# Kernel tuning notes

Measured on AMD Instinct MI355X. Metric: run time of the kernel, lower is better.

## Reference

```python
import jax, jax.numpy as jnp
import numpy as np
import math

HIDDEN = 1024
HEADS = 16
D_K = HIDDEN // HEADS
EPS = 1e-5


def gelu_tanh(x):
    c = math.sqrt(2.0 / math.pi)
    return 0.5 * x * (1.0 + jnp.tanh(c * (x + 0.044715 * x ** 3)))


def layer_norm(x, gamma, beta):
    mu = jnp.mean(x, axis=-1, keepdims=True)
    var = jnp.mean((x - mu) ** 2, axis=-1, keepdims=True)
    return (x - mu) * jax.lax.rsqrt(var + EPS) * gamma + beta


def setup_inputs() -> dict:
    key = jax.random.key(0)
    ks = jax.random.split(key, 12)
    s = 1.0 / math.sqrt(HIDDEN)
    s4 = 1.0 / math.sqrt(4 * HIDDEN)
    inp = {
        "x": jax.random.normal(ks[0], (2, 2048, HIDDEN), dtype=jnp.float32),
        # attention linears, stored as (in, out) so y = x @ W + b
        "Wq": jax.random.uniform(ks[1], (HIDDEN, HIDDEN), minval=-s, maxval=s),
        "bq": jax.random.uniform(ks[2], (HIDDEN,), minval=-s, maxval=s),
        "Wv": jax.random.uniform(ks[3], (HIDDEN, HIDDEN), minval=-s, maxval=s),
        "bv": jax.random.uniform(ks[4], (HIDDEN,), minval=-s, maxval=s),
        "Wo": jax.random.uniform(ks[5], (HIDDEN, HIDDEN), minval=-s, maxval=s),
        "bo": jax.random.uniform(ks[6], (HIDDEN,), minval=-s, maxval=s),
        # feed-forward
        "W1": jax.random.uniform(ks[7], (HIDDEN, 4 * HIDDEN), minval=-s, maxval=s),
        "b1": jax.random.uniform(ks[8], (4 * HIDDEN,), minval=-s, maxval=s),
        "W2": jax.random.uniform(ks[9], (4 * HIDDEN, HIDDEN), minval=-s4, maxval=s4),
        "b2": jax.random.uniform(ks[10], (HIDDEN,), minval=-s4, maxval=s4),
        # layer norms
        "g1": jnp.ones((HIDDEN,), jnp.float32),
        "beta1": jnp.zeros((HIDDEN,), jnp.float32),
        "g2": jnp.ones((HIDDEN,), jnp.float32),
        "beta2": jnp.zeros((HIDDEN,), jnp.float32),
    }
    return inp


def attention(x, Wq, bq, Wv, bv, Wo, bo):
    bs, seq, _ = x.shape
    qk = (x @ Wq + bq).reshape(bs, seq, HEADS, D_K).transpose(0, 2, 1, 3)  # b h s d
    v = (x @ Wv + bv).reshape(bs, seq, HEADS, D_K).transpose(0, 2, 1, 3)
    scores = jnp.einsum('bhqd,bhkd->bhqk', qk, qk) / math.sqrt(D_K)
    causal = jnp.tril(jnp.ones((seq, seq), dtype=bool))
    scores = jnp.where(causal[None, None], scores, -jnp.inf)
    attn = jax.nn.softmax(scores, axis=-1)
    out = jnp.einsum('bhqk,bhkd->bhqd', attn, v)
    out = out.transpose(0, 2, 1, 3).reshape(bs, seq, HIDDEN)
    return out @ Wo + bo


def reference(x, Wq, bq, Wv, bv, Wo, bo, W1, b1, W2, b2, g1, beta1, g2, beta2):
    x = x + attention(layer_norm(x, g1, beta1), Wq, bq, Wv, bv, Wo, bo)
    h = layer_norm(x, g2, beta2)
    ff = gelu_tanh(h @ W1 + b1) @ W2 + b2  # chunking is a memory detail; same math
    return x + ff
```

## Files before the change

### kernel.cpp

```cpp
#include <hip/hip_runtime.h>

typedef unsigned short u16;
typedef short bf16x8 __attribute__((ext_vector_type(8)));
typedef float f32x4 __attribute__((ext_vector_type(4)));

__device__ __forceinline__ float bf2f(u16 u) {
    union { unsigned int i; float f; } v; v.i = ((unsigned int)u) << 16; return v.f;
}
__device__ __forceinline__ u16 f2bf(float f) {
    union { float f; unsigned int i; } v; v.f = f;
    unsigned int r = v.i + 0x7fffu + ((v.i >> 16) & 1u);
    return (u16)(r >> 16);
}

__device__ __forceinline__ void gload16(const u16* g, u16* l) {
    __builtin_amdgcn_global_load_lds((__attribute__((address_space(1))) void*)(u16*)g,
                                     (__attribute__((address_space(3))) void*)l, 16, 0, 0);
}

__global__ __launch_bounds__(256) void prep(const float* __restrict__ Wq,
                                            const float* __restrict__ Wv,
                                            const float* __restrict__ Wo,
                                            const float* __restrict__ W1,
                                            const float* __restrict__ W2,
                                            const float* __restrict__ bq,
                                            const float* __restrict__ bv,
                                            u16* __restrict__ WqT, u16* __restrict__ WvT,
                                            u16* __restrict__ WoT, u16* __restrict__ W1T,
                                            u16* __restrict__ W2T, float* __restrict__ bqv) {
    int id = blockIdx.x;
    if (id >= 2816) {
        int i = (id - 2816) * 256 + threadIdx.x;
        bqv[i] = (i < 1024) ? bq[i] : bv[i - 1024];
        return;
    }
    const float* in; u16* out; int R, C, bx, by;
    if (id < 256)       { in = Wq; out = WqT; R = 1024; C = 1024; bx = id & 15;          by = id >> 4; }
    else if (id < 512)  { int t = id - 256;  in = Wv; out = WvT; R = 1024; C = 1024; bx = t & 15; by = t >> 4; }
    else if (id < 768)  { int t = id - 512;  in = Wo; out = WoT; R = 1024; C = 1024; bx = t & 15; by = t >> 4; }
    else if (id < 1792) { int t = id - 768;  in = W1; out = W1T; R = 1024; C = 4096; bx = t & 63; by = t >> 6; }
    else                { int t = id - 1792; in = W2; out = W2T; R = 4096; C = 1024; bx = t & 15; by = t >> 4; }
    __shared__ u16 tile[64][65];
    int c0 = bx * 64, r0 = by * 64;
    for (int i = threadIdx.x; i < 4096; i += 256) {
        int r = i >> 6, c = i & 63;
        tile[r][c] = f2bf(in[(size_t)(r0 + r) * C + c0 + c]);
    }
    __syncthreads();
    for (int i = threadIdx.x; i < 4096; i += 256) {
        int r = i >> 6, c = i & 63;
        out[(size_t)(c0 + r) * R + r0 + c] = tile[c][r];
    }
}

__global__ __launch_bounds__(256) void transpose_bf16_s(const u16* __restrict__ in,
                                                        u16* __restrict__ out,
                                                        int R, int C, int istride) {
    __shared__ u16 tile[64][65];
    int c0 = blockIdx.x * 64, r0 = blockIdx.y * 64;
    in  += (size_t)blockIdx.z * R * istride;
    out += (size_t)blockIdx.z * R * C;
    for (int i = threadIdx.x; i < 4096; i += 256) {
        int r = i >> 6, c = i & 63;
        tile[r][c] = in[(size_t)(r0 + r) * istride + c0 + c];
    }
    __syncthreads();
    for (int i = threadIdx.x; i < 4096; i += 256) {
        int r = i >> 6, c = i & 63;
        out[(size_t)(c0 + r) * R + r0 + c] = tile[c][r];
    }
}

__global__ __launch_bounds__(256) void ln_f32(const float* __restrict__ x,
                                              const float* __restrict__ g,
                                              const float* __restrict__ be,
                                              u16* __restrict__ out) {
    int row = blockIdx.x, tid = threadIdx.x;
    int lane = tid & 63, wave = tid >> 6;
    const float* xr = x + (size_t)row * 1024 + tid * 4;
    float4 f4 = *(const float4*)xr;
    float v[4] = {f4.x, f4.y, f4.z, f4.w};
    float s1 = v[0] + v[1] + v[2] + v[3];
    float s2 = v[0]*v[0] + v[1]*v[1] + v[2]*v[2] + v[3]*v[3];
#pragma unroll
    for (int mm = 1; mm < 64; mm <<= 1) { s1 += __shfl_xor(s1, mm); s2 += __shfl_xor(s2, mm); }
    __shared__ float a1[4], a2[4];
    if (lane == 0) { a1[wave] = s1; a2[wave] = s2; }
    __syncthreads();
    s1 = a1[0] + a1[1] + a1[2] + a1[3];
    s2 = a2[0] + a2[1] + a2[2] + a2[3];
    float mean = s1 * (1.0f / 1024.0f);
    float var  = s2 * (1.0f / 1024.0f) - mean * mean;
    float rstd = rsqrtf(var + 1e-5f);
#pragma unroll
    for (int i = 0; i < 4; ++i) {
        int c = tid * 4 + i;
        float o = (v[i] - mean) * rstd * g[c] + be[c];
        out[(size_t)row * 1024 + c] = f2bf(o);
    }
}

__global__ __launch_bounds__(256) void ln_bf16(const u16* __restrict__ x,
                                               const float* __restrict__ g,
                                               const float* __restrict__ be,
                                               u16* __restrict__ out) {
    int row = blockIdx.x, tid = threadIdx.x;
    int lane = tid & 63, wave = tid >> 6;
    u16 e[4]; *(uint2*)e = *(const uint2*)(x + (size_t)row * 1024 + tid * 4);
    float v[4];
#pragma unroll
    for (int i = 0; i < 4; ++i) v[i] = bf2f(e[i]);
    float s1 = v[0] + v[1] + v[2] + v[3];
    float s2 = v[0]*v[0] + v[1]*v[1] + v[2]*v[2] + v[3]*v[3];
#pragma unroll
    for (int mm = 1; mm < 64; mm <<= 1) { s1 += __shfl_xor(s1, mm); s2 += __shfl_xor(s2, mm); }
    __shared__ float a1[4], a2[4];
    if (lane == 0) { a1[wave] = s1; a2[wave] = s2; }
    __syncthreads();
    s1 = a1[0] + a1[1] + a1[2] + a1[3];
    s2 = a2[0] + a2[1] + a2[2] + a2[3];
    float mean = s1 * (1.0f / 1024.0f);
    float var  = s2 * (1.0f / 1024.0f) - mean * mean;
    float rstd = rsqrtf(var + 1e-5f);
#pragma unroll
    for (int i = 0; i < 4; ++i) {
        int c = tid * 4 + i;
        float o = (v[i] - mean) * rstd * g[c] + be[c];
        out[(size_t)row * 1024 + c] = f2bf(o);
    }
}

template <int BN, int ACT, int RES, typename OutT>
__global__ __launch_bounds__(256) void gemm_gl(const u16* __restrict__ A,
                                               const u16* __restrict__ WT,
                                               const float* __restrict__ bias,
                                               const float* __restrict__ resid,
                                               OutT* __restrict__ C,
                                               int M, int N, int K, int cpx) {
    constexpr int JN = BN / 32;
    __shared__ u16 lds_a[128 * 64];
    __shared__ u16 lds_b[BN * 64];
    int tid = threadIdx.x;
    int lane = tid & 63, wave = tid >> 6;
    int l16 = lane & 15, quad = lane >> 4;
    int wm = (wave >> 1) * 64, wn = (wave & 1) * (BN / 2);

    int id = blockIdx.x;
    int slot = id >> 3;
    int bx = (id & 7) * cpx + (slot >> 5);
    int by = slot & 31;
    int m0 = by * 128, n0 = bx * BN;
    f32x4 acc[4][JN] = {};

    int scol = ((lane & 7) ^ (lane >> 3)) * 8;
    const u16* Ab = A  + (size_t)(m0 + wave * 8 + (lane >> 3)) * K + scol;
    const u16* Bb = WT + (size_t)(n0 + wave * 8 + (lane >> 3)) * K + scol;
    u16* la = lds_a + wave * 512;
    u16* lb = lds_b + wave * 512;
    int xk = (l16 & 7);

    for (int k0 = 0; k0 < K; k0 += 64) {
        __syncthreads();
#pragma unroll
        for (int it = 0; it < 4; ++it)
            gload16(Ab + (size_t)it * 32 * K + k0, la + it * 2048);
#pragma unroll
        for (int it = 0; it < JN; ++it)
            gload16(Bb + (size_t)it * 32 * K + k0, lb + it * 2048);
        __syncthreads();
#pragma unroll
        for (int s = 0; s < 2; ++s) {
            bf16x8 af[4], bfr[JN];
#pragma unroll
            for (int i = 0; i < 4; ++i)
                af[i] = *(const bf16x8*)&lds_a[(wm + i * 16 + l16) * 64 + (((s * 4 + quad) ^ xk) * 8)];
#pragma unroll
            for (int j = 0; j < JN; ++j)
                bfr[j] = *(const bf16x8*)&lds_b[(wn + j * 16 + l16) * 64 + (((s * 4 + quad) ^ xk) * 8)];
#pragma unroll
            for (int i = 0; i < 4; ++i)
#pragma unroll
                for (int j = 0; j < JN; ++j)
                    acc[i][j] = __builtin_amdgcn_mfma_f32_16x16x32_bf16(af[i], bfr[j], acc[i][j], 0, 0, 0);
        }
    }

#pragma unroll
    for (int j = 0; j < JN; ++j) {
        int col = n0 + wn + j * 16 + l16;
        float bv = bias[col];
#pragma unroll
        for (int i = 0; i < 4; ++i) {
            int rbase = m0 + wm + i * 16 + quad * 4;
#pragma unroll
            for (int r = 0; r < 4; ++r) {
                size_t idx = (size_t)(rbase + r) * N + col;
                float v = acc[i][j][r] + bv;
                if (ACT == 1) {
                    float u = v;
                    float y = 0.7978845608028654f * (u + 0.044715f * u * u * u);
                    float t = __expf(2.0f * y);
                    float th = 1.0f - 2.0f / (t + 1.0f);
                    v = 0.5f * u * (1.0f + th);
                }
                if (RES) v += resid[idx];
                if constexpr (sizeof(OutT) == 4) C[idx] = v;
                else                             C[idx] = f2bf(v);
            }
        }
    }
}

template <int ACT>
__global__ __launch_bounds__(256, 2) void gemm_big(const u16* __restrict__ A,
                                                   const u16* __restrict__ WT,
                                                   const float* __restrict__ bias,
                                                   u16* __restrict__ C,
                                                   int M, int N, int K) {
    __shared__ u16 lds_a[256 * 64];
    __shared__ u16 lds_b[128 * 64];
    int tid = threadIdx.x;
    int lane = tid & 63, wave = tid >> 6;
    int l16 = lane & 15, quad = lane >> 4;
    int wm = (wave >> 1) * 128, wn = (wave & 1) * 64;
    int id = blockIdx.x;
    int bx = id & 31, by = id >> 5;
    int m0 = by * 256, n0 = bx * 128;
    f32x4 acc[8][4] = {};

    int scol = ((lane & 7) ^ (lane >> 3)) * 8;
    const u16* Ab = A  + (size_t)(m0 + wave * 8 + (lane >> 3)) * K + scol;
    const u16* Bb = WT + (size_t)(n0 + wave * 8 + (lane >> 3)) * K + scol;
    u16* la = lds_a + wave * 512;
    u16* lb = lds_b + wave * 512;
    int xk = (l16 & 7);

    for (int k0 = 0; k0 < K; k0 += 64) {
        __syncthreads();
#pragma unroll
        for (int it = 0; it < 8; ++it)
            gload16(Ab + (size_t)it * 32 * K + k0, la + it * 2048);
#pragma unroll
        for (int it = 0; it < 4; ++it)
            gload16(Bb + (size_t)it * 32 * K + k0, lb + it * 2048);
        __syncthreads();
#pragma unroll
        for (int s = 0; s < 2; ++s) {
            bf16x8 bfr[4];
#pragma unroll
            for (int j = 0; j < 4; ++j)
                bfr[j] = *(const bf16x8*)&lds_b[(wn + j * 16 + l16) * 64 + (((s * 4 + quad) ^ xk) * 8)];
#pragma unroll
            for (int i = 0; i < 8; ++i) {
                bf16x8 af = *(const bf16x8*)&lds_a[(wm + i * 16 + l16) * 64 + (((s * 4 + quad) ^ xk) * 8)];
#pragma unroll
                for (int j = 0; j < 4; ++j)
                    acc[i][j] = __builtin_amdgcn_mfma_f32_16x16x32_bf16(af, bfr[j], acc[i][j], 0, 0, 0);
            }
        }
    }

#pragma unroll
    for (int j = 0; j < 4; ++j) {
        int col = n0 + wn + j * 16 + l16;
        float bv = bias[col];
#pragma unroll
        for (int i = 0; i < 8; ++i) {
            int rbase = m0 + wm + i * 16 + quad * 4;
#pragma unroll
            for (int r = 0; r < 4; ++r) {
                size_t idx = (size_t)(rbase + r) * N + col;
                float v = acc[i][j][r] + bv;
                if (ACT == 1) {
                    float u = v;
                    float y = 0.7978845608028654f * (u + 0.044715f * u * u * u);
                    float t = __expf(2.0f * y);
                    float th = 1.0f - 2.0f / (t + 1.0f);
                    v = 0.5f * u * (1.0f + th);
                }
                C[idx] = f2bf(v);
            }
        }
    }
}

__global__ __launch_bounds__(256, 2) void gemm_split(const u16* __restrict__ A,
                                                     const u16* __restrict__ WT,
                                                     u16* __restrict__ p0,
                                                     u16* __restrict__ p1,
                                                     u16* __restrict__ p2,
                                                     int M, int N, int K) {
    __shared__ u16 lds_a[256 * 64];
    __shared__ u16 lds_b[128 * 64];
    int tid = threadIdx.x;
    int lane = tid & 63, wave = tid >> 6;
    int l16 = lane & 15, quad = lane >> 4;
    int wm = (wave >> 1) * 128, wn = (wave & 1) * 64;
    int id = blockIdx.x;
    int slice = id >> 7;
    int t = id & 127;
    int bx = t & 7, by = t >> 3;
    int m0 = by * 256, n0 = bx * 128;
    int k_lo = (slice == 0) ? 0 : 64 * (22 + 21 * (slice - 1));
    int k_hi = (slice == 2) ? K : 64 * (22 + 21 * slice);
    u16* P = (slice == 0) ? p0 : (slice == 1) ? p1 : p2;
    f32x4 acc[8][4] = {};

    int scol = ((lane & 7) ^ (lane >> 3)) * 8;
    const u16* Ab = A  + (size_t)(m0 + wave * 8 + (lane >> 3)) * K + scol;
    const u16* Bb = WT + (size_t)(n0 + wave * 8 + (lane >> 3)) * K + scol;
    u16* la = lds_a + wave * 512;
    u16* lb = lds_b + wave * 512;
    int xk = (l16 & 7);

    for (int k0 = k_lo; k0 < k_hi; k0 += 64) {
        __syncthreads();
#pragma unroll
        for (int it = 0; it < 8; ++it)
            gload16(Ab + (size_t)it * 32 * K + k0, la + it * 2048);
#pragma unroll
        for (int it = 0; it < 4; ++it)
            gload16(Bb + (size_t)it * 32 * K + k0, lb + it * 2048);
        __syncthreads();
#pragma unroll
        for (int s = 0; s < 2; ++s) {
            bf16x8 bfr[4];
#pragma unroll
            for (int j = 0; j < 4; ++j)
                bfr[j] = *(const bf16x8*)&lds_b[(wn + j * 16 + l16) * 64 + (((s * 4 + quad) ^ xk) * 8)];
#pragma unroll
            for (int i = 0; i < 8; ++i) {
                bf16x8 af = *(const bf16x8*)&lds_a[(wm + i * 16 + l16) * 64 + (((s * 4 + quad) ^ xk) * 8)];
#pragma unroll
                for (int j = 0; j < 4; ++j)
                    acc[i][j] = __builtin_amdgcn_mfma_f32_16x16x32_bf16(af, bfr[j], acc[i][j], 0, 0, 0);
            }
        }
    }

#pragma unroll
    for (int j = 0; j < 4; ++j) {
        int col = n0 + wn + j * 16 + l16;
#pragma unroll
        for (int i = 0; i < 8; ++i) {
            int rbase = m0 + wm + i * 16 + quad * 4;
#pragma unroll
            for (int r = 0; r < 4; ++r)
                P[(size_t)(rbase + r) * N + col] = f2bf(acc[i][j][r]);
        }
    }
}

__global__ __launch_bounds__(256) void ff2_reduce(const u16* __restrict__ p0,
                                                  const u16* __restrict__ p1,
                                                  const u16* __restrict__ p2,
                                                  const u16* __restrict__ x2b,
                                                  const float* __restrict__ b2,
                                                  float* __restrict__ out) {
    size_t i = ((size_t)blockIdx.x * 256 + threadIdx.x) * 8;
    int col = (int)(i & 1023);
    uint4 a0 = *(const uint4*)&p0[i];
    uint4 a1 = *(const uint4*)&p1[i];
    uint4 a2 = *(const uint4*)&p2[i];
    uint4 ax = *(const uint4*)&x2b[i];
    const u16* e0 = (const u16*)&a0;
    const u16* e1 = (const u16*)&a1;
    const u16* e2 = (const u16*)&a2;
    const u16* ex = (const u16*)&ax;
    float o[8];
#pragma unroll
    for (int e = 0; e < 8; ++e)
        o[e] = bf2f(ex[e]) + bf2f(e0[e]) + bf2f(e1[e]) + bf2f(e2[e]) + b2[col + e];
    *(float4*)&out[i]     = *(float4*)&o[0];
    *(float4*)&out[i + 4] = *(float4*)&o[4];
}

__global__ __launch_bounds__(256) void attn_kernel(const u16* __restrict__ QV,
                                                   const u16* __restrict__ Vt,
                                                   u16* __restrict__ Out) {
    int id = blockIdx.x;
    int slot = id >> 3;
    int hb = (id & 7) + 8 * (slot & 3);
    int p  = slot >> 2;
    int h = hb & 15, b = hb >> 4;
    int tid = threadIdx.x;
    int lane = tid & 63, wave = tid >> 6;
    int l16 = lane & 15, quad = lane >> 4;

    __shared__ u16 k_lds[64 * 64];
    __shared__ u16 v_lds[64 * 64];
    __shared__ u16 p_lds[4][16 * 72];

    bf16x8 ones;
#pragma unroll
    for (int e = 0; e < 8; ++e) ones[e] = (short)0x3F80;

    int srow = wave * 8 + (lane >> 3);
    int sc8  = ((lane & 7) ^ (lane >> 3)) * 8;
    int xk   = (l16 & 7);

    for (int half = 0; half < 2; ++half) {
        int t = half ? (31 - p) : p;
        int q0 = t * 64;

        const u16* qp = QV + ((size_t)b * 2048 + q0 + wave * 16 + l16) * 2048 + h * 64;
        bf16x8 qf[2];
        qf[0] = *(const bf16x8*)&qp[quad * 8];
        qf[1] = *(const bf16x8*)&qp[32 + quad * 8];

        f32x4 O[4] = {};
        f32x4 L = {};

        for (int kt = 0; kt <= t; ++kt) {
            const u16* kg = QV + ((size_t)b * 2048 + kt * 64 + srow) * 2048 + h * 64 + sc8;
            const u16* vg = Vt + ((((size_t)b * 16 + h) * 64) + srow) * 2048 + kt * 64 + sc8;
            __syncthreads();
            gload16(kg,                      k_lds + wave * 512);
            gload16(kg + (size_t)32 * 2048,  k_lds + wave * 512 + 2048);
            gload16(vg,                      v_lds + wave * 512);
            gload16(vg + (size_t)32 * 2048,  v_lds + wave * 512 + 2048);
            __syncthreads();

            f32x4 S[4] = {};
#pragma unroll
            for (int s = 0; s < 2; ++s)
#pragma unroll
                for (int j = 0; j < 4; ++j) {
                    bf16x8 kf = *(const bf16x8*)&k_lds[(j * 16 + l16) * 64 + (((s * 4 + quad) ^ xk) * 8)];
                    S[j] = __builtin_amdgcn_mfma_f32_16x16x32_bf16(qf[s], kf, S[j], 0, 0, 0);
                }

            if (kt == t) {
#pragma unroll
                for (int j = 0; j < 4; ++j) {
                    int key = j * 16 + l16;
#pragma unroll
                    for (int r = 0; r < 4; ++r)
                        if (key > wave * 16 + quad * 4 + r) S[j][r] = -1e30f;
                }
            }

#pragma unroll
            for (int j = 0; j < 4; ++j)
#pragma unroll
                for (int r = 0; r < 4; ++r) {
                    float pp = __expf(S[j][r] * 0.125f);
                    p_lds[wave][(quad * 4 + r) * 72 + j * 16 + l16] = f2bf(pp);
                }

#pragma unroll
            for (int s = 0; s < 2; ++s) {
                bf16x8 pf = *(const bf16x8*)&p_lds[wave][l16 * 72 + s * 32 + quad * 8];
                L = __builtin_amdgcn_mfma_f32_16x16x32_bf16(pf, ones, L, 0, 0, 0);
#pragma unroll
                for (int dj = 0; dj < 4; ++dj) {
                    bf16x8 vf = *(const bf16x8*)&v_lds[(dj * 16 + l16) * 64 + (((s * 4 + quad) ^ xk) * 8)];
                    O[dj] = __builtin_amdgcn_mfma_f32_16x16x32_bf16(pf, vf, O[dj], 0, 0, 0);
                }
            }
        }

#pragma unroll
        for (int r = 0; r < 4; ++r) {
            int qg = q0 + wave * 16 + quad * 4 + r;
            float inv = 1.0f / L[r];
#pragma unroll
            for (int dj = 0; dj < 4; ++dj)
                Out[((size_t)b * 2048 + qg) * 1024 + h * 64 + dj * 16 + l16] =
                    f2bf(O[dj][r] * inv);
        }
    }
}

extern "C" void kernel_launch(void* const* d_in, const int* in_sizes, int n_in,
                              void* d_out, int out_size, void* d_ws, size_t ws_size,
                              hipStream_t stream) {
    const float* x   = (const float*)d_in[0];
    const float* Wq  = (const float*)d_in[1];
    const float* bq  = (const float*)d_in[2];
    const float* Wv  = (const float*)d_in[3];
    const float* bv  = (const float*)d_in[4];
    const float* Wo  = (const float*)d_in[5];
    const float* bo  = (const float*)d_in[6];
    const float* W1  = (const float*)d_in[7];
    const float* b1  = (const float*)d_in[8];
    const float* W2  = (const float*)d_in[9];
    const float* b2  = (const float*)d_in[10];
    const float* g1  = (const float*)d_in[11];
    const float* be1 = (const float*)d_in[12];
    const float* g2  = (const float*)d_in[13];
    const float* be2 = (const float*)d_in[14];

    char* ws = (char*)d_ws;
    const size_t MB = 1 << 20;
    u16*   WqT  = (u16*)(ws + 0  * MB);
    u16*   WvT  = (u16*)(ws + 2  * MB);
    u16*   WoT  = (u16*)(ws + 4  * MB);
    u16*   W1T  = (u16*)(ws + 6  * MB);
    u16*   W2T  = (u16*)(ws + 14 * MB);
    u16*   h1   = (u16*)(ws + 22 * MB);
    u16*   QV   = (u16*)(ws + 30 * MB);
    u16*   x2b  = (u16*)(ws + 30 * MB);
    u16*   Vt   = (u16*)(ws + 46 * MB);
    u16*   ff1  = (u16*)(ws + 46 * MB);
    float* bqv  = (float*)(ws + 78 * MB);
    u16*   fp0  = (u16*)(ws + 0  * MB);
    u16*   fp1  = (u16*)(ws + 22 * MB);
    u16*   fp2  = (u16*)(ws + 38 * MB);

    prep<<<2824, 256, 0, stream>>>(Wq, Wv, Wo, W1, W2, bq, bv,
                                   WqT, WvT, WoT, W1T, W2T, bqv);

    ln_f32<<<4096, 256, 0, stream>>>(x, g1, be1, h1);

    gemm_gl<64, 0, 0, u16><<<1024, 256, 0, stream>>>(h1, WqT, bqv, nullptr, QV, 4096, 2048, 1024, 4);

    transpose_bf16_s<<<dim3(16, 32, 2), 256, 0, stream>>>(QV + 1024, Vt, 2048, 1024, 2048);

    attn_kernel<<<512, 256, 0, stream>>>(QV, Vt, h1);

    gemm_gl<64, 0, 1, u16><<<512, 256, 0, stream>>>(h1, WoT, bo, x, x2b, 4096, 1024, 1024, 2);

    ln_bf16<<<4096, 256, 0, stream>>>(x2b, g2, be2, h1);

    gemm_big<1><<<512, 256, 0, stream>>>(h1, W1T, b1, ff1, 4096, 4096, 1024);

    gemm_split<<<384, 256, 0, stream>>>(ff1, W2T, fp0, fp1, fp2, 4096, 1024, 4096);

    ff2_reduce<<<2048, 256, 0, stream>>>(fp0, fp1, fp2, x2b, b2, (float*)d_out);
}
```

Measured before the change: 329.3 us.

## Fuse first layernorm into prep, widen QV GEMM tile, split attention per query tile

Moves the first layer norm into the weight-prep kernel as extra blocks, which removes one launch. The Q/V projection GEMM now uses BN=128 tiles with half the grid. Attention gives each block a single query tile instead of a balanced pair, so 1024 blocks run with the heaviest tiles scheduled first. This is meant to raise parallelism and cut launch overhead, at the cost of per-block load imbalance and of the LN work sharing a launch with the transpose blocks.

```diff
diff --git a/kernel.cpp b/kernel.cpp
--- a/kernel.cpp
+++ b/kernel.cpp
@@ -25,12 +25,41 @@
                                             const float* __restrict__ W2,
                                             const float* __restrict__ bq,
                                             const float* __restrict__ bv,
+                                            const float* __restrict__ x,
+                                            const float* __restrict__ g1,
+                                            const float* __restrict__ be1,
                                             u16* __restrict__ WqT, u16* __restrict__ WvT,
                                             u16* __restrict__ WoT, u16* __restrict__ W1T,
-                                            u16* __restrict__ W2T, float* __restrict__ bqv) {
+                                            u16* __restrict__ W2T, float* __restrict__ bqv,
+                                            u16* __restrict__ h1) {
     int id = blockIdx.x;
+    int tid = threadIdx.x;
+    if (id >= 2824) {
+        int row = id - 2824;
+        int lane = tid & 63, wave = tid >> 6;
+        float4 f4 = *(const float4*)(x + (size_t)row * 1024 + tid * 4);
+        float v[4] = {f4.x, f4.y, f4.z, f4.w};
+        float s1 = v[0] + v[1] + v[2] + v[3];
+        float s2 = v[0]*v[0] + v[1]*v[1] + v[2]*v[2] + v[3]*v[3];
+#pragma unroll
+        for (int mm = 1; mm < 64; mm <<= 1) { s1 += __shfl_xor(s1, mm); s2 += __shfl_xor(s2, mm); }
+        __shared__ float a1[4], a2[4];
+        if (lane == 0) { a1[wave] = s1; a2[wave] = s2; }
+        __syncthreads();
+        s1 = a1[0] + a1[1] + a1[2] + a1[3];
+        s2 = a2[0] + a2[1] + a2[2] + a2[3];
+        float mean = s1 * (1.0f / 1024.0f);
+        float var  = s2 * (1.0f / 1024.0f) - mean * mean;
+        float rstd = rsqrtf(var + 1e-5f);
+#pragma unroll
+        for (int i = 0; i < 4; ++i) {
+            int c = tid * 4 + i;
+            h1[(size_t)row * 1024 + c] = f2bf((v[i] - mean) * rstd * g1[c] + be1[c]);
+        }
+        return;
+    }
     if (id >= 2816) {
-        int i = (id - 2816) * 256 + threadIdx.x;
+        int i = (id - 2816) * 256 + tid;
         bqv[i] = (i < 1024) ? bq[i] : bv[i - 1024];
         return;
     }
@@ -42,12 +71,12 @@
     else                { int t = id - 1792; in = W2; out = W2T; R = 4096; C = 1024; bx = t & 15; by = t >> 4; }
     __shared__ u16 tile[64][65];
     int c0 = bx * 64, r0 = by * 64;
-    for (int i = threadIdx.x; i < 4096; i += 256) {
+    for (int i = tid; i < 4096; i += 256) {
         int r = i >> 6, c = i & 63;
         tile[r][c] = f2bf(in[(size_t)(r0 + r) * C + c0 + c]);
     }
     __syncthreads();
-    for (int i = threadIdx.x; i < 4096; i += 256) {
+    for (int i = tid; i < 4096; i += 256) {
         int r = i >> 6, c = i & 63;
         out[(size_t)(c0 + r) * R + r0 + c] = tile[c][r];
     }
@@ -71,15 +100,16 @@
     }
 }
 
-__global__ __launch_bounds__(256) void ln_f32(const float* __restrict__ x,
-                                              const float* __restrict__ g,
-                                              const float* __restrict__ be,
-                                              u16* __restrict__ out) {
+__global__ __launch_bounds__(256) void ln_bf16(const u16* __restrict__ x,
+                                               const float* __restrict__ g,
+                                               const float* __restrict__ be,
+                                               u16* __restrict__ out) {
     int row = blockIdx.x, tid = threadIdx.x;
     int lane = tid & 63, wave = tid >> 6;
-    const float* xr = x + (size_t)row * 1024 + tid * 4;
-    float4 f4 = *(const float4*)xr;
-    float v[4] = {f4.x, f4.y, f4.z, f4.w};
+    u16 e[4]; *(uint2*)e = *(const uint2*)(x + (size_t)row * 1024 + tid * 4);
+    float v[4];
+#pragma unroll
+    for (int i = 0; i < 4; ++i) v[i] = bf2f(e[i]);
     float s1 = v[0] + v[1] + v[2] + v[3];
     float s2 = v[0]*v[0] + v[1]*v[1] + v[2]*v[2] + v[3]*v[3];
 #pragma unroll
@@ -95,38 +125,7 @@
 #pragma unroll
     for (int i = 0; i < 4; ++i) {
         int c = tid * 4 + i;
-        float o = (v[i] - mean) * rstd * g[c] + be[c];
-        out[(size_t)row * 1024 + c] = f2bf(o);
-    }
-}
-
-__global__ __launch_bounds__(256) void ln_bf16(const u16* __restrict__ x,
-                                               const float* __restrict__ g,
-                                               const float* __restrict__ be,
-                                               u16* __restrict__ out) {
-    int row = blockIdx.x, tid = threadIdx.x;
-    int lane = tid & 63, wave = tid >> 6;
-    u16 e[4]; *(uint2*)e = *(const uint2*)(x + (size_t)row * 1024 + tid * 4);
-    float v[4];
-#pragma unroll
-    for (int i = 0; i < 4; ++i) v[i] = bf2f(e[i]);
-    float s1 = v[0] + v[1] + v[2] + v[3];
-    float s2 = v[0]*v[0] + v[1]*v[1] + v[2]*v[2] + v[3]*v[3];
-#pragma unroll
-    for (int mm = 1; mm < 64; mm <<= 1) { s1 += __shfl_xor(s1, mm); s2 += __shfl_xor(s2, mm); }
-    __shared__ float a1[4], a2[4];
-    if (lane == 0) { a1[wave] = s1; a2[wave] = s2; }
-    __syncthreads();
-    s1 = a1[0] + a1[1] + a1[2] + a1[3];
-    s2 = a2[0] + a2[1] + a2[2] + a2[3];
-    float mean = s1 * (1.0f / 1024.0f);
-    float var  = s2 * (1.0f / 1024.0f) - mean * mean;
-    float rstd = rsqrtf(var + 1e-5f);
-#pragma unroll
-    for (int i = 0; i < 4; ++i) {
-        int c = tid * 4 + i;
-        float o = (v[i] - mean) * rstd * g[c] + be[c];
-        out[(size_t)row * 1024 + c] = f2bf(o);
+        out[(size_t)row * 1024 + c] = f2bf((v[i] - mean) * rstd * g[c] + be[c]);
     }
 }
 
@@ -381,7 +380,7 @@
     int id = blockIdx.x;
     int slot = id >> 3;
     int hb = (id & 7) + 8 * (slot & 3);
-    int p  = slot >> 2;
+    int t  = 31 - (slot >> 2);
     int h = hb & 15, b = hb >> 4;
     int tid = threadIdx.x;
     int lane = tid & 63, wave = tid >> 6;
@@ -399,76 +398,72 @@
     int sc8  = ((lane & 7) ^ (lane >> 3)) * 8;
     int xk   = (l16 & 7);
 
-    for (int half = 0; half < 2; ++half) {
-        int t = half ? (31 - p) : p;
-        int q0 = t * 64;
-
-        const u16* qp = QV + ((size_t)b * 2048 + q0 + wave * 16 + l16) * 2048 + h * 64;
-        bf16x8 qf[2];
-        qf[0] = *(const bf16x8*)&qp[quad * 8];
-        qf[1] = *(const bf16x8*)&qp[32 + quad * 8];
-
-        f32x4 O[4] = {};
-        f32x4 L = {};
-
-        for (int kt = 0; kt <= t; ++kt) {
-            const u16* kg = QV + ((size_t)b * 2048 + kt * 64 + srow) * 2048 + h * 64 + sc8;
-            const u16* vg = Vt + ((((size_t)b * 16 + h) * 64) + srow) * 2048 + kt * 64 + sc8;
-            __syncthreads();
-            gload16(kg,                      k_lds + wave * 512);
-            gload16(kg + (size_t)32 * 2048,  k_lds + wave * 512 + 2048);
-            gload16(vg,                      v_lds + wave * 512);
-            gload16(vg + (size_t)32 * 2048,  v_lds + wave * 512 + 2048);
-            __syncthreads();
-
-            f32x4 S[4] = {};
-#pragma unroll
-            for (int s = 0; s < 2; ++s)
-#pragma unroll
-                for (int j = 0; j < 4; ++j) {
-                    bf16x8 kf = *(const bf16x8*)&k_lds[(j * 16 + l16) * 64 + (((s * 4 + quad) ^ xk) * 8)];
-                    S[j] = __builtin_amdgcn_mfma_f32_16x16x32_bf16(qf[s], kf, S[j], 0, 0, 0);
-                }
-
-            if (kt == t) {
-#pragma unroll
-                for (int j = 0; j < 4; ++j) {
-                    int key = j * 16 + l16;
-#pragma unroll
-                    for (int r = 0; r < 4; ++r)
-                        if (key > wave * 16 + quad * 4 + r) S[j][r] = -1e30f;
-                }
-            }
-
-#pragma unroll
-            for (int j = 0; j < 4; ++j)
-#pragma unroll
-                for (int r = 0; r < 4; ++r) {
-                    float pp = __expf(S[j][r] * 0.125f);
-                    p_lds[wave][(quad * 4 + r) * 72 + j * 16 + l16] = f2bf(pp);
-                }
-
-#pragma unroll
-            for (int s = 0; s < 2; ++s) {
-                bf16x8 pf = *(const bf16x8*)&p_lds[wave][l16 * 72 + s * 32 + quad * 8];
-                L = __builtin_amdgcn_mfma_f32_16x16x32_bf16(pf, ones, L, 0, 0, 0);
-#pragma unroll
-                for (int dj = 0; dj < 4; ++dj) {
-                    bf16x8 vf = *(const bf16x8*)&v_lds[(dj * 16 + l16) * 64 + (((s * 4 + quad) ^ xk) * 8)];
-                    O[dj] = __builtin_amdgcn_mfma_f32_16x16x32_bf16(pf, vf, O[dj], 0, 0, 0);
-                }
-            }
-        }
-
-#pragma unroll
-        for (int r = 0; r < 4; ++r) {
-            int qg = q0 + wave * 16 + quad * 4 + r;
-            float inv = 1.0f / L[r];
-#pragma unroll
-            for (int dj = 0; dj < 4; ++dj)
-                Out[((size_t)b * 2048 + qg) * 1024 + h * 64 + dj * 16 + l16] =
-                    f2bf(O[dj][r] * inv);
-        }
+    int q0 = t * 64;
+    const u16* qp = QV + ((size_t)b * 2048 + q0 + wave * 16 + l16) * 2048 + h * 64;
+    bf16x8 qf[2];
+    qf[0] = *(const bf16x8*)&qp[quad * 8];
+    qf[1] = *(const bf16x8*)&qp[32 + quad * 8];
+
+    f32x4 O[4] = {};
+    f32x4 L = {};
+
+    for (int kt = 0; kt <= t; ++kt) {
+        const u16* kg = QV + ((size_t)b * 2048 + kt * 64 + srow) * 2048 + h * 64 + sc8;
+        const u16* vg = Vt + ((((size_t)b * 16 + h) * 64) + srow) * 2048 + kt * 64 + sc8;
+        __syncthreads();
+        gload16(kg,                      k_lds + wave * 512);
+        gload16(kg + (size_t)32 * 2048,  k_lds + wave * 512 + 2048);
+        gload16(vg,                      v_lds + wave * 512);
+        gload16(vg + (size_t)32 * 2048,  v_lds + wave * 512 + 2048);
+        __syncthreads();
+
+        f32x4 S[4] = {};
+#pragma unroll
+        for (int s = 0; s < 2; ++s)
+#pragma unroll
+            for (int j = 0; j < 4; ++j) {
+                bf16x8 kf = *(const bf16x8*)&k_lds[(j * 16 + l16) * 64 + (((s * 4 + quad) ^ xk) * 8)];
+                S[j] = __builtin_amdgcn_mfma_f32_16x16x32_bf16(qf[s], kf, S[j], 0, 0, 0);
+            }
+
+        if (kt == t) {
+#pragma unroll
+            for (int j = 0; j < 4; ++j) {
+                int key = j * 16 + l16;
+#pragma unroll
+                for (int r = 0; r < 4; ++r)
+                    if (key > wave * 16 + quad * 4 + r) S[j][r] = -1e30f;
+            }
+        }
+
+#pragma unroll
+        for (int j = 0; j < 4; ++j)
+#pragma unroll
+            for (int r = 0; r < 4; ++r) {
+                float pp = __expf(S[j][r] * 0.125f);
+                p_lds[wave][(quad * 4 + r) * 72 + j * 16 + l16] = f2bf(pp);
+            }
+
+#pragma unroll
+        for (int s = 0; s < 2; ++s) {
+            bf16x8 pf = *(const bf16x8*)&p_lds[wave][l16 * 72 + s * 32 + quad * 8];
+            L = __builtin_amdgcn_mfma_f32_16x16x32_bf16(pf, ones, L, 0, 0, 0);
+#pragma unroll
+            for (int dj = 0; dj < 4; ++dj) {
+                bf16x8 vf = *(const bf16x8*)&v_lds[(dj * 16 + l16) * 64 + (((s * 4 + quad) ^ xk) * 8)];
+                O[dj] = __builtin_amdgcn_mfma_f32_16x16x32_bf16(pf, vf, O[dj], 0, 0, 0);
+            }
+        }
+    }
+
+#pragma unroll
+    for (int r = 0; r < 4; ++r) {
+        int qg = q0 + wave * 16 + quad * 4 + r;
+        float inv = 1.0f / L[r];
+#pragma unroll
+        for (int dj = 0; dj < 4; ++dj)
+            Out[((size_t)b * 2048 + qg) * 1024 + h * 64 + dj * 16 + l16] =
+                f2bf(O[dj][r] * inv);
     }
 }
 
@@ -508,16 +503,14 @@
     u16*   fp1  = (u16*)(ws + 22 * MB);
     u16*   fp2  = (u16*)(ws + 38 * MB);
 
-    prep<<<2824, 256, 0, stream>>>(Wq, Wv, Wo, W1, W2, bq, bv,
-                                   WqT, WvT, WoT, W1T, W2T, bqv);
-
-    ln_f32<<<4096, 256, 0, stream>>>(x, g1, be1, h1);
-
-    gemm_gl<64, 0, 0, u16><<<1024, 256, 0, stream>>>(h1, WqT, bqv, nullptr, QV, 4096, 2048, 1024, 4);
+    prep<<<6920, 256, 0, stream>>>(Wq, Wv, Wo, W1, W2, bq, bv, x, g1, be1,
+                                   WqT, WvT, WoT, W1T, W2T, bqv, h1);
+
+    gemm_gl<128, 0, 0, u16><<<512, 256, 0, stream>>>(h1, WqT, bqv, nullptr, QV, 4096, 2048, 1024, 2);
 
     transpose_bf16_s<<<dim3(16, 32, 2), 256, 0, stream>>>(QV + 1024, Vt, 2048, 1024, 2048);
 
-    attn_kernel<<<512, 256, 0, stream>>>(QV, Vt, h1);
+    attn_kernel<<<1024, 256, 0, stream>>>(QV, Vt, h1);
 
     gemm_gl<64, 0, 1, u16><<<512, 256, 0, stream>>>(h1, WoT, bo, x, x2b, 4096, 1024, 1024, 2);
 
```

After: 319.0 us. 1.03x faster.
